# Kernel optimization log

Measured on AMD Instinct MI355X. Metric: run time of the kernel, lower is better.

Reference implementation:

```python
import jax, jax.numpy as jnp
import numpy as np

EPS = 1e-8


def _conv1d(x, w, b):
    # x: [B, E, L], w: [F, E, K], b: [F] -> [B, F, L] (k=3, pad=1 keeps length)
    y = jax.lax.conv_general_dilated(
        x, w, window_strides=(1,), padding=[(1, 1)],
        dimension_numbers=("NCH", "OIH", "NCH"))
    return y + b[None, :, None]


def setup_inputs() -> dict:
    key = jax.random.key(0)
    kq, ka, ke, kw, kb, ku = jax.random.split(key, 6)
    B, QL, AL = 512, 128, 512
    V, E, F, K = 50000, 300, 400, 3
    question = jax.random.randint(kq, (B, QL), 0, V + 1, dtype=jnp.int64)
    answer = jax.random.randint(ka, (B, AL), 0, V + 1, dtype=jnp.int64)
    emb_table = jax.random.normal(ke, (V + 1, E), dtype=jnp.float32)
    emb_table = emb_table.at[0].set(0.0)  # padding_idx=0
    conv_w = jax.random.normal(kw, (F, E, K), dtype=jnp.float32) * 0.05
    conv_b = jax.random.normal(kb, (F,), dtype=jnp.float32) * 0.05
    U = jax.random.normal(ku, (F, F), dtype=jnp.float32) * 0.1
    return {"question": question, "answer": answer, "emb_table": emb_table,
            "conv_w": conv_w, "conv_b": conv_b, "U": U}


def reference(question, answer, emb_table, conv_w, conv_b, U):
    q = emb_table[question]              # [B, QL, E]
    a = emb_table[answer]                # [B, AL, E]
    Q = _conv1d(q.transpose(0, 2, 1), conv_w, conv_b)   # [B, F, QL]
    A = _conv1d(a.transpose(0, 2, 1), conv_w, conv_b)   # [B, F, AL]
    # G = tanh(Q^T U A): [B, QL, AL]
    G = jnp.tanh(jnp.einsum("bfq,fg,bga->bqa", Q, U, A))
    roQ = jax.nn.softmax(jnp.max(G, axis=2), axis=1)    # [B, QL]
    roA = jax.nn.softmax(jnp.max(G, axis=1), axis=1)    # [B, AL]
    rQ = jnp.einsum("bfq,bq->bf", Q, roQ)               # [B, F]
    rA = jnp.einsum("bfa,ba->bf", A, roA)               # [B, F]
    nQ = jnp.maximum(jnp.linalg.norm(rQ, axis=1), EPS)
    nA = jnp.maximum(jnp.linalg.norm(rA, axis=1), EPS)
    return jnp.sum(rQ * rA, axis=1) / (nQ * nA)         # [B]
```

## Files before the change

### kernel.cpp

```cpp
#include <hip/hip_runtime.h>
#include <math.h>

typedef unsigned int   uint32;
typedef unsigned short ushort16;
typedef __attribute__((ext_vector_type(8))) short  short8;
typedef __attribute__((ext_vector_type(4))) float  floatx4;

#define Bb   512
#define QLn  128
#define ALn  512
#define En   300
#define Fn   400
#define OW   416
#define EPAD 320
#define NV   50001
#define ECROWS 50176
#define ECSTRIDE 2560

typedef const __attribute__((address_space(1))) unsigned int guint_t;
typedef __attribute__((address_space(3))) unsigned int luint_t;
#define GLDS16(g, l) __builtin_amdgcn_global_load_lds((guint_t*)(g), (luint_t*)(l), 16, 0, 0)

static __device__ __forceinline__ float bf_lo(uint32 u) { return __uint_as_float(u << 16); }
static __device__ __forceinline__ float bf_hi(uint32 u) { return __uint_as_float(u & 0xffff0000u); }
static __device__ __forceinline__ ushort16 f2bf(float f) {
    uint32 u = __float_as_uint(f);
    uint32 r = (u + 0x7fffu + ((u >> 16) & 1u)) >> 16;
    return (ushort16)r;
}
static __device__ __forceinline__ uint32 pack2(float a, float b) {
    return (uint32)f2bf(a) | ((uint32)f2bf(b) << 16);
}

__global__ __launch_bounds__(128) void embcvt_kernel(
        const float* __restrict__ emb, char* __restrict__ embbf)
{
    const int r = blockIdx.x, j = threadIdx.x;
    const float* er = emb + (size_t)r * En;
    uint32* orow = (uint32*)(embbf + (size_t)r * 640);
    for (int d = j; d < 160; d += 128) {
        uint32 v = 0;
        if (d < 150) {
            float2 f2v = *(const float2*)(er + 2 * d);
            v = pack2(f2v.x, f2v.y);
        }
        orow[d] = v;
    }
}

__global__ __launch_bounds__(256) void prep_wt(
        const float* __restrict__ W, const float* __restrict__ cb,
        ushort16* __restrict__ Wt2, float* __restrict__ bias2)
{
    const int f = blockIdx.x, t = threadIdx.x;
    for (int p2 = t; p2 < 480; p2 += 256) {
        int p = 2 * p2;
        float v0 = 0.f, v1 = 0.f;
        if (f < Fn) {
            int kk = p / EPAD, e = p - kk * EPAD;
            if (e < En)     v0 = W[(size_t)f * 900 + e * 3 + kk];
            if (e + 1 < En) v1 = W[(size_t)f * 900 + (e + 1) * 3 + kk];
        }
        *(uint32*)&Wt2[(size_t)f * 960 + p] = pack2(v0, v1);
    }
    if (t == 0) bias2[f] = (f < Fn) ? cb[f] : 0.f;
}

__global__ __launch_bounds__(256) void prep_ub(
        const float* __restrict__ U, ushort16* __restrict__ Ub)
{
    const int g = blockIdx.x, t = threadIdx.x;
    uint32* orow = (uint32*)(Ub + (size_t)g * 416);
    for (int f2 = t; f2 < 208; f2 += 256) {
        int f = 2 * f2;
        float v0 = 0.f, v1 = 0.f;
        if (g < Fn) {
            if (f < Fn)     v0 = U[(size_t)f * Fn + g];
            if (f + 1 < Fn) v1 = U[(size_t)(f + 1) * Fn + g];
        }
        orow[f2] = pack2(v0, v1);
    }
}

__global__ __launch_bounds__(512) void ec_gemm(
        const char* __restrict__ embbf, const char* __restrict__ Wt2,
        char* __restrict__ EC)
{
    __shared__ __align__(16) char As[32768];
    __shared__ __align__(16) char Bs[32768];
    const int t = threadIdx.x, lane = t & 63, w = t >> 6;
    const int v0 = blockIdx.x * 256, c0 = blockIdx.y * 256;
    const int wr = w >> 2, wc = w & 3;
    const int fm = lane & 15;
    const int cg = ((lane & 3) - ((lane >> 3) & 3)) & 3;
    const int rl = lane >> 2;
    const int chunkOff = (((lane >> 4) + (fm >> 1)) & 3) * 16;

    const char* srcA[2];
    const char* srcB[2];
#pragma unroll
    for (int i = 0; i < 2; ++i) {
        srcA[i] = embbf + (size_t)(v0 + w * 32 + i * 16 + rl) * 640 + cg * 16;
        int n = c0 + w * 32 + i * 16 + rl;
        int kk = n / 416, f = n - kk * 416;
        if (n >= 1248) { kk = 0; f = 508; }
        srcB[i] = Wt2 + (size_t)f * 1920 + kk * 640 + cg * 16;
    }
    char* AsW = As + w * 2048;
    char* BsW = Bs + w * 2048;

    floatx4 acc[8][4];
    const floatx4 zz = {0.f, 0.f, 0.f, 0.f};
#pragma unroll
    for (int m = 0; m < 8; ++m)
#pragma unroll
        for (int n = 0; n < 4; ++n) acc[m][n] = zz;

#define ESTG(ko, buf) do {                                                    \
        const int _ko = (ko); const int _bo = (buf) * 16384;                  \
        GLDS16(srcA[0] + _ko, AsW + _bo);                                     \
        GLDS16(srcA[1] + _ko, AsW + _bo + 1024);                              \
        GLDS16(srcB[0] + _ko, BsW + _bo);                                     \
        GLDS16(srcB[1] + _ko, BsW + _bo + 1024);                              \
    } while (0)

    int cur = 0;
    ESTG(0, 0);
    __syncthreads();
    for (int ks = 0; ks < 10; ++ks) {
        const int nxt = cur ^ 1;
        if (ks < 9) ESTG((ks + 1) * 64, nxt);
        short8 af[8], bfv[4];
        const char* Ac = As + cur * 16384;
        const char* Bc = Bs + cur * 16384;
#pragma unroll
        for (int m = 0; m < 8; ++m)
            af[m] = *(const short8*)(Ac + (wr * 128 + m * 16 + fm) * 64 + chunkOff);
#pragma unroll
        for (int n = 0; n < 4; ++n)
            bfv[n] = *(const short8*)(Bc + (wc * 64 + n * 16 + fm) * 64 + chunkOff);
        __builtin_amdgcn_s_setprio(1);
#pragma unroll
        for (int m = 0; m < 8; ++m)
#pragma unroll
            for (int n = 0; n < 4; ++n)
                acc[m][n] = __builtin_amdgcn_mfma_f32_16x16x32_bf16(
                    af[m], bfv[n], acc[m][n], 0, 0, 0);
        __builtin_amdgcn_s_setprio(0);
        __syncthreads();
        cur = nxt;
    }
#undef ESTG

#pragma unroll
    for (int m = 0; m < 8; ++m) {
        const int v = v0 + wr * 128 + m * 16 + ((lane >> 4) * 4);
#pragma unroll
        for (int n = 0; n < 4; ++n) {
            const int col = c0 + wc * 64 + n * 16 + fm;
#pragma unroll
            for (int r = 0; r < 4; ++r)
                *(ushort16*)(EC + (size_t)(v + r) * ECSTRIDE + col * 2) =
                    f2bf(acc[m][n][r]);
        }
    }
}

static __device__ __forceinline__ void gather_one(
        const int* __restrict__ toks, const char* __restrict__ EC,
        const float* __restrict__ bias2, char* __restrict__ outb,
        int id, int L)
{
    const uint32 uid = (uint32)id;
    const int c = (int)(uid % 52u);
    const int r = (int)(uid / 52u);
    const int l = r & (L - 1), b = r / L;
    const int* tr = toks + (size_t)b * L;
    const int t0 = (l > 0)     ? tr[l - 1] : 0;
    const int t1 = tr[l];
    const int t2 = (l < L - 1) ? tr[l + 1] : 0;
    const uint4 x0 = *(const uint4*)(EC + (size_t)t0 * ECSTRIDE +        c * 16);
    const uint4 x1 = *(const uint4*)(EC + (size_t)t1 * ECSTRIDE +  832 + c * 16);
    const uint4 x2 = *(const uint4*)(EC + (size_t)t2 * ECSTRIDE + 1664 + c * 16);
    const float4 b0 = *(const float4*)(bias2 + c * 8);
    const float4 b1 = *(const float4*)(bias2 + c * 8 + 4);
    uint4 o;
    o.x = pack2(bf_lo(x0.x) + bf_lo(x1.x) + bf_lo(x2.x) + b0.x,
                bf_hi(x0.x) + bf_hi(x1.x) + bf_hi(x2.x) + b0.y);
    o.y = pack2(bf_lo(x0.y) + bf_lo(x1.y) + bf_lo(x2.y) + b0.z,
                bf_hi(x0.y) + bf_hi(x1.y) + bf_hi(x2.y) + b0.w);
    o.z = pack2(bf_lo(x0.z) + bf_lo(x1.z) + bf_lo(x2.z) + b1.x,
                bf_hi(x0.z) + bf_hi(x1.z) + bf_hi(x2.z) + b1.y);
    o.w = pack2(bf_lo(x0.w) + bf_lo(x1.w) + bf_lo(x2.w) + b1.z,
                bf_hi(x0.w) + bf_hi(x1.w) + bf_hi(x2.w) + b1.w);
    *(uint4*)(outb + (size_t)r * 832 + c * 16) = o;
}

#define GQB 1024
#define GAB 4096
__global__ __launch_bounds__(256) void gather_both(
        const int* __restrict__ question, const int* __restrict__ answer,
        const char* __restrict__ EC, const float* __restrict__ bias2,
        char* __restrict__ qb, char* __restrict__ ab, int nb)
{
    const int bx = blockIdx.x, t = threadIdx.x;
    if (bx < GQB) {
        const int total = nb * QLn * 52;
        for (int id = bx * 256 + t; id < total; id += GQB * 256)
            gather_one(question, EC, bias2, qb, id, QLn);
    } else {
        const int total = nb * ALn * 52;
        for (int id = (bx - GQB) * 256 + t; id < total; id += GAB * 256)
            gather_one(answer, EC, bias2, ab, id, ALn);
    }
}

template<int NWM, int NWN, int MF, int NF, int BR>
static __device__ __forceinline__ void qp_tile(
        const char* __restrict__ Qb, const char* __restrict__ Ub,
        char* __restrict__ ob, int col0, char* As, char* Bs)
{
    const int t = threadIdx.x, lane = t & 63, w = t >> 6;
    const int wr = w / NWN, wc = w % NWN;
    const int fm = lane & 15;
    const int cg = ((lane & 3) - ((lane >> 3) & 3)) & 3;
    const int rl = lane >> 2;
    const int chunkOff = (((lane >> 4) + (fm >> 1)) & 3) * 16;

    const char* srcA = Qb + (size_t)(w * 16 + rl) * 832 + cg * 16;
    const char* srcB0; const char* srcB1 = 0;
    if (BR == 256) {
        srcB0 = Ub + (size_t)(col0 + w * 32 + rl) * 832 + cg * 16;
        srcB1 = srcB0 + (size_t)16 * 832;
    } else {
        srcB0 = Ub + (size_t)(col0 + w * 16 + rl) * 832 + cg * 16;
        srcB1 = Ub + (size_t)(col0 + 128 + w * 16 + rl) * 832 + cg * 16;
    }
    char* AsW = As + w * 1024;
    char* BsW0; char* BsW1;
    if (BR == 256) { BsW0 = Bs + w * 2048; BsW1 = BsW0 + 1024; }
    else           { BsW0 = Bs + w * 1024; BsW1 = Bs + 8192 + w * 1024; }
    const int BUFB = BR * 64;

    floatx4 acc[MF][NF];
    const floatx4 zz = {0.f, 0.f, 0.f, 0.f};
#pragma unroll
    for (int m = 0; m < MF; ++m)
#pragma unroll
        for (int n = 0; n < NF; ++n) acc[m][n] = zz;

#define QSTG(ko, buf) do {                                                    \
        const int _ko = (ko);                                                 \
        GLDS16(srcA + _ko, AsW + (buf) * 8192);                               \
        GLDS16(srcB0 + _ko, BsW0 + (buf) * BUFB);                             \
        if (BR == 256 || w < 2) GLDS16(srcB1 + _ko, BsW1 + (buf) * BUFB);     \
    } while (0)

    int cur = 0;
    QSTG(0, 0);
    __syncthreads();
    for (int ks = 0; ks < 13; ++ks) {
        const int nxt = cur ^ 1;
        if (ks < 12) QSTG((ks + 1) * 64, nxt);
        short8 af[MF], bfv[NF];
        const char* Ac = As + cur * 8192;
        const char* Bc = Bs + cur * BUFB;
#pragma unroll
        for (int m = 0; m < MF; ++m)
            af[m] = *(const short8*)(Ac + (wr * (MF * 16) + m * 16 + fm) * 64 + chunkOff);
#pragma unroll
        for (int n = 0; n < NF; ++n)
            bfv[n] = *(const short8*)(Bc + (wc * (NF * 16) + n * 16 + fm) * 64 + chunkOff);
        __builtin_amdgcn_s_setprio(1);
#pragma unroll
        for (int m = 0; m < MF; ++m)
#pragma unroll
            for (int n = 0; n < NF; ++n)
                acc[m][n] = __builtin_amdgcn_mfma_f32_16x16x32_bf16(
                    af[m], bfv[n], acc[m][n], 0, 0, 0);
        __builtin_amdgcn_s_setprio(0);
        __syncthreads();
        cur = nxt;
    }
#undef QSTG

#pragma unroll
    for (int m = 0; m < MF; ++m) {
        const int row = wr * (MF * 16) + m * 16 + ((lane >> 4) * 4);
#pragma unroll
        for (int n = 0; n < NF; ++n) {
            const int col = col0 + wc * (NF * 16) + n * 16 + fm;
#pragma unroll
            for (int r = 0; r < 4; ++r)
                *(ushort16*)(ob + (size_t)(row + r) * 832 + col * 2) =
                    f2bf(acc[m][n][r]);
        }
    }
}

__global__ __launch_bounds__(512) void qp_gemm(
        const char* __restrict__ qb, const char* __restrict__ Ub,
        char* __restrict__ qpb, int nb)
{
    __shared__ __align__(16) char As[16384];
    __shared__ __align__(16) char Bs[32768];
    const int bx = blockIdx.x;
    const int xcd = bx & 7, rest = bx >> 3;
    const int nt = rest & 1, b = (rest >> 1) * 8 + xcd;
    if (b >= nb) return;
    const char* Qb = qb + (size_t)b * 106496;
    char* ob = qpb + (size_t)b * 106496;
    if (nt == 0)
        qp_tile<2, 4, 4, 4, 256>(Qb, Ub, ob, 0, As, Bs);
    else
        qp_tile<4, 2, 2, 5, 160>(Qb, Ub, ob, 256, As, Bs);
}

__global__ __launch_bounds__(256) void fused_g(
        const ushort16* __restrict__ Qp,
        const ushort16* __restrict__ Av,
        float* __restrict__ rowPart,
        float* __restrict__ colMg,
        int nb)
{
    __shared__ __align__(16) char Qs[8192];
    __shared__ __align__(16) char Asl[32768];
    __shared__ float rowM4[64][4];

    const int t = threadIdx.x, lane = t & 63, w = t >> 6;
    const int bx = blockIdx.x;
    const int xcd = bx & 7, rest = bx >> 3;
    const int c = rest & 1, mh = (rest >> 1) & 1, b = (rest >> 2) * 8 + xcd;
    if (b >= nb) return;
    const int fm = lane & 15;
    const int cg = ((lane & 3) - ((lane >> 3) & 3)) & 3;
    const int rl = lane >> 2;
    const int chunkOff = (((lane >> 4) + (fm >> 1)) & 3) * 16;

    const char* Qpb = (const char*)Qp + (size_t)b * 106496 + (size_t)mh * 64 * 832;
    const char* Ab  = (const char*)Av + (size_t)b * 425984 + (size_t)c * 212992;
    const char* srcQ  = Qpb + (size_t)(w * 16 + rl) * 832 + cg * 16;
    const char* srcA0 = Ab  + (size_t)(w * 64 + rl) * 832 + cg * 16;

    floatx4 acc[4][4];
    const floatx4 zz = {0.f, 0.f, 0.f, 0.f};
#pragma unroll
    for (int m = 0; m < 4; ++m)
#pragma unroll
        for (int n = 0; n < 4; ++n) acc[m][n] = zz;

#define FSTG(ko, buf) do {                                                    \
        const int _ko = (ko);                                                 \
        GLDS16(srcQ + _ko,          Qs  + (buf) * 4096  + w * 1024);          \
        GLDS16(srcA0 + _ko,         Asl + (buf) * 16384 + w * 4096);          \
        GLDS16(srcA0 + 13312 + _ko, Asl + (buf) * 16384 + w * 4096 + 1024);   \
        GLDS16(srcA0 + 26624 + _ko, Asl + (buf) * 16384 + w * 4096 + 2048);   \
        GLDS16(srcA0 + 39936 + _ko, Asl + (buf) * 16384 + w * 4096 + 3072);   \
    } while (0)

    int cur = 0;
    FSTG(0, 0);
    __syncthreads();

    for (int ks = 0; ks < 13; ++ks) {
        const int nxt = cur ^ 1;
        if (ks < 12) FSTG((ks + 1) * 64, nxt);

        short8 qa[4], aa_[4];
        const char* Qc = Qs + cur * 4096;
        const char* Ac = Asl + cur * 16384;
#pragma unroll
        for (int m = 0; m < 4; ++m)
            qa[m] = *(const short8*)(Qc + (m * 16 + fm) * 64 + chunkOff);
#pragma unroll
        for (int n = 0; n < 4; ++n)
            aa_[n] = *(const short8*)(Ac + (w * 64 + n * 16 + fm) * 64 + chunkOff);
        __builtin_amdgcn_s_setprio(1);
#pragma unroll
        for (int m = 0; m < 4; ++m)
#pragma unroll
            for (int n = 0; n < 4; ++n)
                acc[m][n] = __builtin_amdgcn_mfma_f32_16x16x32_bf16(
                    qa[m], aa_[n], acc[m][n], 0, 0, 0);
        __builtin_amdgcn_s_setprio(0);
        __syncthreads();
        cur = nxt;
    }
#undef FSTG

#pragma unroll
    for (int m = 0; m < 4; ++m)
#pragma unroll
        for (int r = 0; r < 4; ++r) {
            float v = fmaxf(fmaxf(acc[m][0][r], acc[m][1][r]),
                            fmaxf(acc[m][2][r], acc[m][3][r]));
            v = fmaxf(v, __shfl_xor(v, 1));
            v = fmaxf(v, __shfl_xor(v, 2));
            v = fmaxf(v, __shfl_xor(v, 4));
            v = fmaxf(v, __shfl_xor(v, 8));
            if (fm == 0) rowM4[m * 16 + (lane >> 4) * 4 + r][w] = v;
        }
#pragma unroll
    for (int n = 0; n < 4; ++n) {
        float v = -1e30f;
#pragma unroll
        for (int m = 0; m < 4; ++m)
#pragma unroll
            for (int r = 0; r < 4; ++r) v = fmaxf(v, acc[m][n][r]);
        v = fmaxf(v, __shfl_xor(v, 16));
        v = fmaxf(v, __shfl_xor(v, 32));
        if (lane < 16)
            colMg[((size_t)b * 2 + mh) * 512 + c * 256 + w * 64 + n * 16 + lane] = v;
    }
    __syncthreads();
    if (t < 64)
        rowPart[((size_t)b * 2 + c) * 128 + mh * 64 + t] =
            fmaxf(fmaxf(rowM4[t][0], rowM4[t][1]),
                  fmaxf(rowM4[t][2], rowM4[t][3]));
}

static __device__ __forceinline__ float red_max_512(float v, volatile float* red) {
    int t = threadIdx.x;
    red[t] = v; __syncthreads();
    for (int s = 256; s > 0; s >>= 1) {
        if (t < s) red[t] = fmaxf(red[t], red[t + s]);
        __syncthreads();
    }
    float r = red[0]; __syncthreads();
    return r;
}
static __device__ __forceinline__ float red_sum_512(float v, volatile float* red) {
    int t = threadIdx.x;
    red[t] = v; __syncthreads();
    for (int s = 256; s > 0; s >>= 1) {
        if (t < s) red[t] = red[t] + red[t + s];
        __syncthreads();
    }
    float r = red[0]; __syncthreads();
    return r;
}

__global__ __launch_bounds__(512) void pool_a(
        const ushort16* __restrict__ Qv,
        const ushort16* __restrict__ Av,
        const float* __restrict__ rowPart,
        const float* __restrict__ colMg,
        float* __restrict__ scratch,
        int nb)
{
    __shared__ float colv[ALn];
    __shared__ float roq[QLn];
    __shared__ float red[512];
    __shared__ float part[2][4][208];
    const int t = threadIdx.x, bx = blockIdx.x;
    const int qtr = bx & 3, b = bx >> 2;

    float v = -1e30f;
    if (t < QLn) {
        const float* rp = rowPart + (size_t)b * 256;
        v = tanhf(fmaxf(rp[t], rp[128 + t]));
    }
    float vmax = red_max_512(v, red);
    float ex = (t < QLn) ? __expf(v - vmax) : 0.f;
    float ssum = red_sum_512(ex, red);
    if (t < QLn) roq[t] = ex / ssum;

    const float* cm = colMg + (size_t)b * 1024;
    float cv = tanhf(fmaxf(cm[t], cm[512 + t]));
    float cmax = red_max_512(cv, red);
    float e0 = __expf(cv - cmax);
    float csum = red_sum_512(e0, red);
    colv[t] = e0 / csum;
    __syncthreads();

    if (t < 416) {
        const int half = t / 208, c = t - half * 208;
        float rq0 = 0.f, rq1 = 0.f, ra0 = 0.f, ra1 = 0.f;
        const uint32* Qb32 = (const uint32*)((const char*)Qv + (size_t)b * 106496);
        const int q0r = qtr * 32 + half * 16;
#pragma unroll 4
        for (int q = q0r; q < q0r + 16; ++q) {
            float wv = roq[q];
            uint32 u = Qb32[q * 208 + c];
            rq0 = fmaf(bf_lo(u), wv, rq0);
            rq1 = fmaf(bf_hi(u), wv, rq1);
        }
        const uint32* Ab32 = (const uint32*)((const char*)Av + (size_t)b * 425984);
        const int a0r = qtr * 128 + half * 64;
#pragma unroll 4
        for (int a = a0r; a < a0r + 64; ++a) {
            float wv = colv[a];
            uint32 u = Ab32[a * 208 + c];
            ra0 = fmaf(bf_lo(u), wv, ra0);
            ra1 = fmaf(bf_hi(u), wv, ra1);
        }
        part[half][0][c] = rq0; part[half][1][c] = rq1;
        part[half][2][c] = ra0; part[half][3][c] = ra1;
    }
    __syncthreads();

    if (t < 208) {
        float* sc = scratch + ((size_t)b * 4 + qtr) * 832;
        sc[t]       = part[0][0][t] + part[1][0][t];
        sc[208 + t] = part[0][1][t] + part[1][1][t];
        sc[416 + t] = part[0][2][t] + part[1][2][t];
        sc[624 + t] = part[0][3][t] + part[1][3][t];
    }
}

static __device__ __forceinline__ float red_sum_256(float v, volatile float* red) {
    int t = threadIdx.x;
    red[t] = v; __syncthreads();
    for (int s = 128; s > 0; s >>= 1) {
        if (t < s) red[t] = red[t] + red[t + s];
        __syncthreads();
    }
    float r = red[0]; __syncthreads();
    return r;
}

__global__ __launch_bounds__(256) void pool_b(
        const float* __restrict__ scratch, float* __restrict__ out, int nb)
{
    __shared__ float red[256];
    const int t = threadIdx.x, b = blockIdx.x;
    float dd = 0.f, qq = 0.f, aam = 0.f;
    if (t < 208) {
        float q0 = 0.f, q1 = 0.f, a0 = 0.f, a1 = 0.f;
#pragma unroll
        for (int qtr = 0; qtr < 4; ++qtr) {
            const float* sc = scratch + ((size_t)b * 4 + qtr) * 832;
            q0 += sc[t]; q1 += sc[208 + t];
            a0 += sc[416 + t]; a1 += sc[624 + t];
        }
        dd  = q0 * a0 + q1 * a1;
        qq  = q0 * q0 + q1 * q1;
        aam = a0 * a0 + a1 * a1;
    }
    dd  = red_sum_256(dd, red);
    qq  = red_sum_256(qq, red);
    aam = red_sum_256(aam, red);
    if (t == 0) {
        float nq = fmaxf(sqrtf(qq), 1e-8f);
        float na = fmaxf(sqrtf(aam), 1e-8f);
        out[b] = dd / (nq * na);
    }
}

extern "C" void kernel_launch(void* const* d_in, const int* in_sizes, int n_in,
                              void* d_out, int out_size, void* d_ws, size_t ws_size,
                              hipStream_t stream)
{
    const int*   question = (const int*)d_in[0];
    const int*   answer   = (const int*)d_in[1];
    const float* emb      = (const float*)d_in[2];
    const float* conv_w   = (const float*)d_in[3];
    const float* conv_b   = (const float*)d_in[4];
    const float* U        = (const float*)d_in[5];
    float* out = (float*)d_out;
    char* ws = (char*)d_ws;

    const size_t WT2B   = (size_t)512 * 960 * 2;
    const size_t UBB    = (size_t)416 * 416 * 2;
    const size_t ECB    = (size_t)ECROWS * ECSTRIDE;
    const size_t FIXED0 = WT2B + 2048 + UBB + ECB;
    const size_t QB     = (size_t)QLn * OW * 2;
    const size_t AB     = (size_t)ALn * OW * 2;
    const size_t MXB    = 20480;
    const size_t PER_B  = 2 * QB + AB + MXB;

    size_t avail = (ws_size > FIXED0) ? (ws_size - FIXED0) : 0;
    int CB = (int)(avail / PER_B);
    if (CB > Bb) CB = Bb;
    if (CB < 1)  CB = 1;
    int nch = (Bb + CB - 1) / CB;
    int CBe = (Bb + nch - 1) / nch;

    char*  wt2   = ws;
    float* bias2 = (float*)(ws + WT2B);
    char*  ub    = ws + WT2B + 2048;
    char*  EC    = ws + WT2B + 2048 + UBB;
    char*  embbf = ws + FIXED0;
    char*  qb    = ws + FIXED0;
    char*  qpb   = qb  + (size_t)CB * QB;
    char*  ab    = qpb + (size_t)CB * QB;
    float* rowP  = (float*)(ab + (size_t)CB * AB);
    float* colM  = rowP + (size_t)CB * 256;
    float* scr   = colM + (size_t)CB * 1024;

    embcvt_kernel<<<NV, 128, 0, stream>>>(emb, embbf);
    prep_wt<<<512, 256, 0, stream>>>(conv_w, conv_b, (ushort16*)wt2, bias2);
    prep_ub<<<416, 256, 0, stream>>>(U, (ushort16*)ub);
    ec_gemm<<<dim3(196, 5), 512, 0, stream>>>(embbf, wt2, EC);

    for (int b0 = 0; b0 < Bb; b0 += CBe) {
        int nb = (Bb - b0 < CBe) ? (Bb - b0) : CBe;
        int nb8 = (nb + 7) / 8;
        gather_both<<<GQB + GAB, 256, 0, stream>>>(
            question + (size_t)b0 * QLn, answer + (size_t)b0 * ALn,
            EC, bias2, qb, ab, nb);
        qp_gemm<<<nb8 * 16, 512, 0, stream>>>(qb, ub, qpb, nb);
        fused_g<<<nb8 * 32, 256, 0, stream>>>((const ushort16*)qpb, (const ushort16*)ab,
                                              rowP, colM, nb);
        pool_a<<<nb * 4, 512, 0, stream>>>((const ushort16*)qb, (const ushort16*)ab,
                                           rowP, colM, scr, nb);
        pool_b<<<nb, 256, 0, stream>>>(scr, out + b0, nb);
    }
}
```

Measured before the change: 568.0 us.

## Split Q·U GEMM into 64-row halves and fold pool_b into next gather

The Q·U projection GEMM now runs 256-thread blocks, each covering a 64-row half of the question tile, which doubles the block count and halves the A-tile shared memory. The final pool_b reduction for each chunk moves into extra blocks of the next chunk's gather kernel, and only the last chunk keeps a separate pool_b launch. This aims to raise occupancy and parallelism in the GEMM and to remove one kernel launch per chunk. In exchange, the U tile is now reloaded by twice as many blocks, and the pooling work is interleaved with gather traffic.

```diff
diff --git a/kernel.cpp b/kernel.cpp
--- a/kernel.cpp
+++ b/kernel.cpp
@@ -196,51 +196,93 @@
     *(uint4*)(outb + (size_t)r * 832 + c * 16) = o;
 }
 
+static __device__ __forceinline__ float red_sum_256(float v, volatile float* red) {
+    int t = threadIdx.x;
+    red[t] = v; __syncthreads();
+    for (int s = 128; s > 0; s >>= 1) {
+        if (t < s) red[t] = red[t] + red[t + s];
+        __syncthreads();
+    }
+    float r = red[0]; __syncthreads();
+    return r;
+}
+
+static __device__ __forceinline__ void pool_b_body(
+        const float* __restrict__ scratch, float* __restrict__ out,
+        int b, volatile float* red)
+{
+    const int t = threadIdx.x;
+    float dd = 0.f, qq = 0.f, aam = 0.f;
+    if (t < 208) {
+        float q0 = 0.f, q1 = 0.f, a0 = 0.f, a1 = 0.f;
+#pragma unroll
+        for (int qtr = 0; qtr < 4; ++qtr) {
+            const float* sc = scratch + ((size_t)b * 4 + qtr) * 832;
+            q0 += sc[t]; q1 += sc[208 + t];
+            a0 += sc[416 + t]; a1 += sc[624 + t];
+        }
+        dd  = q0 * a0 + q1 * a1;
+        qq  = q0 * q0 + q1 * q1;
+        aam = a0 * a0 + a1 * a1;
+    }
+    dd  = red_sum_256(dd, red);
+    qq  = red_sum_256(qq, red);
+    aam = red_sum_256(aam, red);
+    if (t == 0) {
+        float nq = fmaxf(sqrtf(qq), 1e-8f);
+        float na = fmaxf(sqrtf(aam), 1e-8f);
+        out[b] = dd / (nq * na);
+    }
+}
+
 #define GQB 1024
 #define GAB 4096
 __global__ __launch_bounds__(256) void gather_both(
         const int* __restrict__ question, const int* __restrict__ answer,
         const char* __restrict__ EC, const float* __restrict__ bias2,
-        char* __restrict__ qb, char* __restrict__ ab, int nb)
-{
+        char* __restrict__ qb, char* __restrict__ ab, int nb,
+        const float* __restrict__ scrPrev, float* __restrict__ outPrev,
+        int nbPrev)
+{
+    __shared__ float red[256];
     const int bx = blockIdx.x, t = threadIdx.x;
     if (bx < GQB) {
         const int total = nb * QLn * 52;
         for (int id = bx * 256 + t; id < total; id += GQB * 256)
             gather_one(question, EC, bias2, qb, id, QLn);
-    } else {
+    } else if (bx < GQB + GAB) {
         const int total = nb * ALn * 52;
         for (int id = (bx - GQB) * 256 + t; id < total; id += GAB * 256)
             gather_one(answer, EC, bias2, ab, id, ALn);
-    }
-}
-
-template<int NWM, int NWN, int MF, int NF, int BR>
-static __device__ __forceinline__ void qp_tile(
+    } else {
+        const int b = bx - GQB - GAB;
+        if (b < nbPrev) pool_b_body(scrPrev, outPrev, b, red);
+    }
+}
+
+template<int MF, int NF, int BR>
+static __device__ __forceinline__ void qp_tile64(
         const char* __restrict__ Qb, const char* __restrict__ Ub,
         char* __restrict__ ob, int col0, char* As, char* Bs)
 {
     const int t = threadIdx.x, lane = t & 63, w = t >> 6;
+    const int NWN = (MF == 4) ? 4 : 2;
     const int wr = w / NWN, wc = w % NWN;
     const int fm = lane & 15;
     const int cg = ((lane & 3) - ((lane >> 3) & 3)) & 3;
     const int rl = lane >> 2;
     const int chunkOff = (((lane >> 4) + (fm >> 1)) & 3) * 16;
-
-    const char* srcA = Qb + (size_t)(w * 16 + rl) * 832 + cg * 16;
-    const char* srcB0; const char* srcB1 = 0;
+    const int BUFB = BR * 64;
+
+    const char* srcQ = Qb + (size_t)(w * 16 + rl) * 832 + cg * 16;
+    const char* srcB0;
+    const char* srcB1 = 0;
     if (BR == 256) {
+        srcB0 = Ub + (size_t)(col0 + w * 64 + rl) * 832 + cg * 16;
+    } else {
         srcB0 = Ub + (size_t)(col0 + w * 32 + rl) * 832 + cg * 16;
-        srcB1 = srcB0 + (size_t)16 * 832;
-    } else {
-        srcB0 = Ub + (size_t)(col0 + w * 16 + rl) * 832 + cg * 16;
         srcB1 = Ub + (size_t)(col0 + 128 + w * 16 + rl) * 832 + cg * 16;
     }
-    char* AsW = As + w * 1024;
-    char* BsW0; char* BsW1;
-    if (BR == 256) { BsW0 = Bs + w * 2048; BsW1 = BsW0 + 1024; }
-    else           { BsW0 = Bs + w * 1024; BsW1 = Bs + 8192 + w * 1024; }
-    const int BUFB = BR * 64;
 
     floatx4 acc[MF][NF];
     const floatx4 zz = {0.f, 0.f, 0.f, 0.f};
@@ -251,9 +293,17 @@
 
 #define QSTG(ko, buf) do {                                                    \
         const int _ko = (ko);                                                 \
-        GLDS16(srcA + _ko, AsW + (buf) * 8192);                               \
-        GLDS16(srcB0 + _ko, BsW0 + (buf) * BUFB);                             \
-        if (BR == 256 || w < 2) GLDS16(srcB1 + _ko, BsW1 + (buf) * BUFB);     \
+        GLDS16(srcQ + _ko, As + (buf) * 4096 + w * 1024);                     \
+        if (BR == 256) {                                                      \
+            GLDS16(srcB0 + _ko,         Bs + (buf) * BUFB + w * 4096);        \
+            GLDS16(srcB0 + 13312 + _ko, Bs + (buf) * BUFB + w * 4096 + 1024); \
+            GLDS16(srcB0 + 26624 + _ko, Bs + (buf) * BUFB + w * 4096 + 2048); \
+            GLDS16(srcB0 + 39936 + _ko, Bs + (buf) * BUFB + w * 4096 + 3072); \
+        } else {                                                              \
+            GLDS16(srcB0 + _ko,         Bs + (buf) * BUFB + w * 2048);        \
+            GLDS16(srcB0 + 13312 + _ko, Bs + (buf) * BUFB + w * 2048 + 1024); \
+            if (w < 2) GLDS16(srcB1 + _ko, Bs + (buf) * BUFB + 8192 + w * 1024); \
+        }                                                                     \
     } while (0)
 
     int cur = 0;
@@ -263,7 +313,7 @@
         const int nxt = cur ^ 1;
         if (ks < 12) QSTG((ks + 1) * 64, nxt);
         short8 af[MF], bfv[NF];
-        const char* Ac = As + cur * 8192;
+        const char* Ac = As + cur * 4096;
         const char* Bc = Bs + cur * BUFB;
 #pragma unroll
         for (int m = 0; m < MF; ++m)
@@ -298,22 +348,22 @@
     }
 }
 
-__global__ __launch_bounds__(512) void qp_gemm(
+__global__ __launch_bounds__(256) void qp_gemm(
         const char* __restrict__ qb, const char* __restrict__ Ub,
         char* __restrict__ qpb, int nb)
 {
-    __shared__ __align__(16) char As[16384];
+    __shared__ __align__(16) char As[8192];
     __shared__ __align__(16) char Bs[32768];
     const int bx = blockIdx.x;
     const int xcd = bx & 7, rest = bx >> 3;
-    const int nt = rest & 1, b = (rest >> 1) * 8 + xcd;
+    const int nt = rest & 1, mh = (rest >> 1) & 1, b = (rest >> 2) * 8 + xcd;
     if (b >= nb) return;
-    const char* Qb = qb + (size_t)b * 106496;
-    char* ob = qpb + (size_t)b * 106496;
+    const char* Qb = qb + (size_t)b * 106496 + (size_t)mh * 64 * 832;
+    char* ob = qpb + (size_t)b * 106496 + (size_t)mh * 64 * 832;
     if (nt == 0)
-        qp_tile<2, 4, 4, 4, 256>(Qb, Ub, ob, 0, As, Bs);
+        qp_tile64<4, 4, 256>(Qb, Ub, ob, 0, As, Bs);
     else
-        qp_tile<4, 2, 2, 5, 160>(Qb, Ub, ob, 256, As, Bs);
+        qp_tile64<2, 5, 160>(Qb, Ub, ob, 256, As, Bs);
 }
 
 __global__ __launch_bounds__(256) void fused_g(
@@ -508,43 +558,11 @@
     }
 }
 
-static __device__ __forceinline__ float red_sum_256(float v, volatile float* red) {
-    int t = threadIdx.x;
-    red[t] = v; __syncthreads();
-    for (int s = 128; s > 0; s >>= 1) {
-        if (t < s) red[t] = red[t] + red[t + s];
-        __syncthreads();
-    }
-    float r = red[0]; __syncthreads();
-    return r;
-}
-
 __global__ __launch_bounds__(256) void pool_b(
         const float* __restrict__ scratch, float* __restrict__ out, int nb)
 {
     __shared__ float red[256];
-    const int t = threadIdx.x, b = blockIdx.x;
-    float dd = 0.f, qq = 0.f, aam = 0.f;
-    if (t < 208) {
-        float q0 = 0.f, q1 = 0.f, a0 = 0.f, a1 = 0.f;
-#pragma unroll
-        for (int qtr = 0; qtr < 4; ++qtr) {
-            const float* sc = scratch + ((size_t)b * 4 + qtr) * 832;
-            q0 += sc[t]; q1 += sc[208 + t];
-            a0 += sc[416 + t]; a1 += sc[624 + t];
-        }
-        dd  = q0 * a0 + q1 * a1;
-        qq  = q0 * q0 + q1 * q1;
-        aam = a0 * a0 + a1 * a1;
-    }
-    dd  = red_sum_256(dd, red);
-    qq  = red_sum_256(qq, red);
-    aam = red_sum_256(aam, red);
-    if (t == 0) {
-        float nq = fmaxf(sqrtf(qq), 1e-8f);
-        float na = fmaxf(sqrtf(aam), 1e-8f);
-        out[b] = dd / (nq * na);
-    }
+    pool_b_body(scratch, out, blockIdx.x, red);
 }
 
 extern "C" void kernel_launch(void* const* d_in, const int* in_sizes, int n_in,
@@ -593,17 +611,21 @@
     prep_ub<<<416, 256, 0, stream>>>(U, (ushort16*)ub);
     ec_gemm<<<dim3(196, 5), 512, 0, stream>>>(embbf, wt2, EC);
 
+    int prevNb = 0;
+    float* prevOut = out;
     for (int b0 = 0; b0 < Bb; b0 += CBe) {
         int nb = (Bb - b0 < CBe) ? (Bb - b0) : CBe;
         int nb8 = (nb + 7) / 8;
-        gather_both<<<GQB + GAB, 256, 0, stream>>>(
+        gather_both<<<GQB + GAB + prevNb, 256, 0, stream>>>(
             question + (size_t)b0 * QLn, answer + (size_t)b0 * ALn,
-            EC, bias2, qb, ab, nb);
-        qp_gemm<<<nb8 * 16, 512, 0, stream>>>(qb, ub, qpb, nb);
+            EC, bias2, qb, ab, nb, scr, prevOut, prevNb);
+        qp_gemm<<<nb8 * 32, 256, 0, stream>>>(qb, ub, qpb, nb);
         fused_g<<<nb8 * 32, 256, 0, stream>>>((const ushort16*)qpb, (const ushort16*)ab,
                                               rowP, colM, nb);
         pool_a<<<nb * 4, 512, 0, stream>>>((const ushort16*)qb, (const ushort16*)ab,
                                            rowP, colM, scr, nb);
-        pool_b<<<nb, 256, 0, stream>>>(scr, out + b0, nb);
-    }
-}
+        prevNb = nb;
+        prevOut = out + b0;
+    }
+    pool_b<<<prevNb, 256, 0, stream>>>(scr, prevOut, prevNb);
+}
```

Result: no change. 559.1 us (-1.6%).
